# Kernel tuning notes

Measured on AMD Instinct MI355X. Metric: run time of the kernel, lower is better.

## Reference

```python
import jax, jax.numpy as jnp
import numpy as np

B, T, I, H, O = 64, 2048, 128, 512, 128


def setup_inputs() -> dict:
    key = jax.random.key(0)
    ks = jax.random.split(key, 9)
    sI = 1.0 / np.sqrt(I)
    sH = 1.0 / np.sqrt(H)
    return {
        "x": jax.random.normal(ks[0], (B, T, I), jnp.float32),
        "h0": jnp.zeros((1, B, H), jnp.float32),
        "W_ih": jax.random.normal(ks[1], (H, I), jnp.float32) * sI,
        "b_ih": jax.random.normal(ks[2], (H,), jnp.float32) * sH,
        "W_hh": jax.random.normal(ks[3], (H, H), jnp.float32) * sH,
        "b_hh": jax.random.normal(ks[4], (H,), jnp.float32) * sH,
        "mask_ih": (jax.random.uniform(ks[5], (H, I)) < 0.8).astype(jnp.float32),
        "mask_hh": (jax.random.uniform(ks[6], (H, H)) < 0.8).astype(jnp.float32),
        "W_fc": jax.random.normal(ks[7], (O, H), jnp.float32) * sH,
        "b_fc": jax.random.normal(ks[8], (O,), jnp.float32) * sH,
    }


def reference(x, h0, W_ih, b_ih, W_hh, b_hh, mask_ih, mask_hh, W_fc, b_fc):
    # Masked weights (mask applied once, outside the time loop)
    Wih_m = W_ih * mask_ih          # [H, I]
    Whh_m = W_hh * mask_hh          # [H, H]

    # Precompute the input projection for all timesteps: [T, B, H]
    xt = jnp.swapaxes(x, 0, 1)      # time-major for scan
    xproj = jnp.einsum("tbi,hi->tbh", xt, Wih_m) + b_ih + b_hh

    def step(h, xp_t):
        # Elman RNN cell with tanh nonlinearity (torch nn.RNN default)
        h_new = jnp.tanh(xp_t + h @ Whh_m.T)
        return h_new, h_new

    _, hs = jax.lax.scan(step, h0[0], xproj)   # hs: [T, B, H]

    # Linear readout over all timesteps, back to batch_first
    out = jnp.einsum("tbh,oh->tbo", hs, W_fc) + b_fc
    return jnp.swapaxes(out, 0, 1)             # [B, T, O]
```

## Files before the change

### kernel.cpp

```cpp
#include <hip/hip_runtime.h>

typedef unsigned int u32;
typedef _Float16 half_t;
typedef _Float16 half2_t __attribute__((ext_vector_type(2)));

#define B_ 64
#define T_ 2048
#define I_ 128
#define H_ 512
#define O_ 128

static __device__ __forceinline__ float dot2w(u32 w, u32 h, float acc) {
  return __builtin_amdgcn_fdot2(__builtin_bit_cast(half2_t, w),
                                __builtin_bit_cast(half2_t, h), acc, false);
}

__global__ void k_prep(const float* __restrict__ Whh, const float* __restrict__ Mhh,
                       const float* __restrict__ Wih, const float* __restrict__ Mih,
                       const float* __restrict__ Wfc,
                       u32* __restrict__ Whh_pk, u32* __restrict__ Wih_pk,
                       u32* __restrict__ Wfc_pk) {
  int idx = blockIdx.x * 256 + threadIdx.x;
  if (idx < 512 * 256) {
    int w4 = idx >> 11;
    int rem = idx & 2047;
    int l = rem >> 2;
    int c = rem & 3;
    int q = w4 * 4 + c;
    int j = q >> 5;
    int m = q & 31;
    int row = (l >> 3) * 8 + j;
    int k0 = (l & 7) * 64 + m * 2;
    float a = Whh[row * 512 + k0]     * Mhh[row * 512 + k0];
    float b = Whh[row * 512 + k0 + 1] * Mhh[row * 512 + k0 + 1];
    half2_t hv = { (half_t)a, (half_t)b };
    Whh_pk[idx] = __builtin_bit_cast(u32, hv);
  } else if (idx < 512 * 256 + 512 * 64) {
    int i2 = idx - 512 * 256;
    int h = i2 >> 6, w = i2 & 63;
    int k0 = w * 2;
    float a = Wih[h * 128 + k0]     * Mih[h * 128 + k0];
    float b = Wih[h * 128 + k0 + 1] * Mih[h * 128 + k0 + 1];
    half2_t hv = { (half_t)a, (half_t)b };
    Wih_pk[h * 64 + w] = __builtin_bit_cast(u32, hv);
  } else if (idx < 512 * 256 + 512 * 64 + 128 * 256) {
    int i3 = idx - (512 * 256 + 512 * 64);
    int o = i3 >> 8, w = i3 & 255;
    float a = Wfc[o * 512 + 2 * w];
    float b = Wfc[o * 512 + 2 * w + 1];
    half2_t hv = { (half_t)a, (half_t)b };
    Wfc_pk[o * 256 + w] = __builtin_bit_cast(u32, hv);
  }
}

__launch_bounds__(512, 2)
__global__ void k_xproj(const float* __restrict__ x, const u32* __restrict__ Wih_pk,
                        const float* __restrict__ b_ih, const float* __restrict__ b_hh,
                        half_t* __restrict__ xp) {
  const int l = threadIdx.x;
  const int r0 = blockIdx.x * 256;
  __shared__ u32 xb[2][64];
  u32 W[64];
#pragma unroll
  for (int i = 0; i < 16; ++i)
    *(uint4*)&W[i * 4] = *(const uint4*)(Wih_pk + l * 64 + i * 4);
  const float bs = b_ih[l] + b_hh[l];

  float2 g = { 0.f, 0.f };
  if (l < 64) {
    g = *(const float2*)(x + (size_t)r0 * 128 + 2 * l);
    half2_t hv = { (half_t)g.x, (half_t)g.y };
    xb[0][l] = __builtin_bit_cast(u32, hv);
    g = *(const float2*)(x + (size_t)(r0 + 1) * 128 + 2 * l);
  }
  __syncthreads();
  for (int i = 0; i < 256; ++i) {
    if (l < 64 && i + 1 < 256) {
      half2_t hv = { (half_t)g.x, (half_t)g.y };
      xb[(i + 1) & 1][l] = __builtin_bit_cast(u32, hv);
      int nf = (i + 2 < 256) ? i + 2 : i + 1;
      g = *(const float2*)(x + (size_t)(r0 + nf) * 128 + 2 * l);
    }
    float a0 = 0.f, a1 = 0.f;
#pragma unroll
    for (int m = 0; m < 16; ++m) {
      uint4 hv = *(const uint4*)&xb[i & 1][m * 4];
      a0 = dot2w(W[m * 4 + 0], hv.x, a0);
      a1 = dot2w(W[m * 4 + 1], hv.y, a1);
      a0 = dot2w(W[m * 4 + 2], hv.z, a0);
      a1 = dot2w(W[m * 4 + 3], hv.w, a1);
    }
    xp[(size_t)(r0 + i) * 512 + l] = (half_t)(a0 + a1 + bs);
    __syncthreads();
  }
}

__launch_bounds__(512, 2)
__global__ void k_rec(const u32* __restrict__ Whh_pk, half_t* __restrict__ xp,
                      const float* __restrict__ h0) {
  const int b = blockIdx.x;
  const int l = threadIdx.x;
  const int g = l & 7;
  const int row = l;

  __shared__ u32 hbuf[2][288];
  __shared__ u32 wlds[512 * 52];

  u32 W[208];
#pragma unroll
  for (int w4 = 0; w4 < 64; ++w4) {
    uint4 v = *(const uint4*)(Whh_pk + (size_t)w4 * 2048 + l * 4);
    const int j = w4 >> 3, p = w4 & 7;
    if (j < 4) {
      if (p < 7) {
        W[j * 28 + p * 4 + 0] = v.x; W[j * 28 + p * 4 + 1] = v.y;
        W[j * 28 + p * 4 + 2] = v.z; W[j * 28 + p * 4 + 3] = v.w;
      } else {
        *(uint4*)&wlds[l * 52 + j * 4] = v;
      }
    } else {
      if (p < 6) {
        int base = 112 + (j - 4) * 24 + p * 4;
        W[base + 0] = v.x; W[base + 1] = v.y; W[base + 2] = v.z; W[base + 3] = v.w;
      } else {
        *(uint4*)&wlds[l * 52 + 16 + (j - 4) * 8 + (p - 6) * 4] = v;
      }
    }
  }
  if (l < 256) {
    float2 hv = *(const float2*)(h0 + (size_t)b * 512 + 2 * l);
    half2_t hh = { (half_t)hv.x, (half_t)hv.y };
    hbuf[0][l + (l >> 5) * 4] = __builtin_bit_cast(u32, hh);
  }
  __syncthreads();

  half_t* xpb = xp + (size_t)b * T_ * 512 + row;
  half_t xp0 = xpb[0];
  half_t xp1 = xpb[512];

  const int b0 = l & 1, b1 = (l >> 1) & 1, b2 = (l >> 2) & 1;
  const int hwIdx = (row >> 1) + (row >> 6) * 4;
  int cur = 0;

  for (int t = 0; t < T_; ++t) {
    int tpf = (t + 2 < T_) ? t + 2 : T_ - 1;
    half_t xpn = xpb[(size_t)tpf * 512];

    float acc[8];
#pragma unroll
    for (int j = 0; j < 8; ++j) acc[j] = 0.f;

#pragma unroll
    for (int m4 = 0; m4 < 8; ++m4) {
      uint4 hh = *(const uint4*)&hbuf[cur][g * 36 + m4 * 4];
#pragma unroll
      for (int j = 0; j < 8; ++j) {
        u32 w0, w1, w2, w3;
        if (j < 4) {
          if (m4 < 7) {
            w0 = W[j * 28 + m4 * 4 + 0]; w1 = W[j * 28 + m4 * 4 + 1];
            w2 = W[j * 28 + m4 * 4 + 2]; w3 = W[j * 28 + m4 * 4 + 3];
          } else {
            uint4 wv = *(const uint4*)&wlds[l * 52 + j * 4];
            w0 = wv.x; w1 = wv.y; w2 = wv.z; w3 = wv.w;
          }
        } else {
          if (m4 < 6) {
            int base = 112 + (j - 4) * 24 + m4 * 4;
            w0 = W[base + 0]; w1 = W[base + 1]; w2 = W[base + 2]; w3 = W[base + 3];
          } else {
            uint4 wv = *(const uint4*)&wlds[l * 52 + 16 + (j - 4) * 8 + (m4 - 6) * 4];
            w0 = wv.x; w1 = wv.y; w2 = wv.z; w3 = wv.w;
          }
        }
        acc[j] = dot2w(w0, hh.x, acc[j]);
        acc[j] = dot2w(w1, hh.y, acc[j]);
        acc[j] = dot2w(w2, hh.z, acc[j]);
        acc[j] = dot2w(w3, hh.w, acc[j]);
      }
    }

    float s4[4];
#pragma unroll
    for (int m = 0; m < 4; ++m) {
      float keep = b0 ? acc[2 * m + 1] : acc[2 * m];
      float send = b0 ? acc[2 * m]     : acc[2 * m + 1];
      s4[m] = keep + __shfl_xor(send, 1, 64);
    }
    float s2[2];
#pragma unroll
    for (int m = 0; m < 2; ++m) {
      float keep = b1 ? s4[2 * m + 1] : s4[2 * m];
      float send = b1 ? s4[2 * m]     : s4[2 * m + 1];
      s2[m] = keep + __shfl_xor(send, 2, 64);
    }
    float keepf = b2 ? s2[1] : s2[0];
    float sendf = b2 ? s2[0] : s2[1];
    float tot = keepf + __shfl_xor(sendf, 4, 64);

    float sarg = tot + (float)xp0;
    float ax = fabsf(sarg);
    float e = __expf(-2.f * ax);
    float r = (1.f - e) * __builtin_amdgcn_rcpf(1.f + e);
    float hval = copysignf(r, sarg);

    half_t hv = (half_t)hval;
    ((half_t*)hbuf[cur ^ 1])[hwIdx * 2 + (row & 1)] = hv;
    xpb[(size_t)t * 512] = hv;

    xp0 = xp1; xp1 = xpn;
    __syncthreads();
    cur ^= 1;
  }
}

__launch_bounds__(256, 2)
__global__ void k_fc(const half_t* __restrict__ hs, const u32* __restrict__ Wfc_pk,
                     const float* __restrict__ b_fc, float* __restrict__ out) {
  const int l = threadIdx.x;
  const int w = l >> 6;
  const int o = (l & 31) + w * 32;
  const int kh = (l >> 5) & 1;
  const int r0 = blockIdx.x * 256;
  __shared__ u32 sb[2][256];
  u32 W[128];
#pragma unroll
  for (int i = 0; i < 32; ++i)
    *(uint4*)&W[i * 4] = *(const uint4*)(Wfc_pk + o * 256 + kh * 128 + i * 4);
  const float bf = b_fc[o];
  const u32* hsw = (const u32*)hs;

  u32 gA = hsw[(size_t)r0 * 256 + l];
  sb[0][l] = gA;
  gA = hsw[(size_t)(r0 + 1) * 256 + l];
  __syncthreads();
  for (int i = 0; i < 256; ++i) {
    if (i + 1 < 256) {
      sb[(i + 1) & 1][l] = gA;
      int nf = (i + 2 < 256) ? i + 2 : i + 1;
      gA = hsw[(size_t)(r0 + nf) * 256 + l];
    }
    float a0 = 0.f, a1 = 0.f;
#pragma unroll
    for (int m = 0; m < 32; ++m) {
      uint4 hv = *(const uint4*)&sb[i & 1][kh * 128 + m * 4];
      a0 = dot2w(W[m * 4 + 0], hv.x, a0);
      a1 = dot2w(W[m * 4 + 1], hv.y, a1);
      a0 = dot2w(W[m * 4 + 2], hv.z, a0);
      a1 = dot2w(W[m * 4 + 3], hv.w, a1);
    }
    float a = a0 + a1;
    a += __shfl_xor(a, 32, 64);
    if (kh == 0) out[(size_t)(r0 + i) * 128 + o] = a + bf;
    __syncthreads();
  }
}

extern "C" void kernel_launch(void* const* d_in, const int* in_sizes, int n_in,
                              void* d_out, int out_size, void* d_ws, size_t ws_size,
                              hipStream_t stream) {
  const float* x   = (const float*)d_in[0];
  const float* h0  = (const float*)d_in[1];
  const float* Wih = (const float*)d_in[2];
  const float* bih = (const float*)d_in[3];
  const float* Whh = (const float*)d_in[4];
  const float* bhh = (const float*)d_in[5];
  const float* Mih = (const float*)d_in[6];
  const float* Mhh = (const float*)d_in[7];
  const float* Wfc = (const float*)d_in[8];
  const float* bfc = (const float*)d_in[9];
  float* out = (float*)d_out;

  char* ws = (char*)d_ws;
  half_t* xproj = (half_t*)(ws);
  u32* Whh_pk = (u32*)(ws + 134217728);
  u32* Wih_pk = (u32*)(ws + 134217728 + 524288);
  u32* Wfc_pk = (u32*)(ws + 134217728 + 524288 + 131072);

  hipLaunchKernelGGL(k_prep, dim3(768), dim3(256), 0, stream,
                     Whh, Mhh, Wih, Mih, Wfc, Whh_pk, Wih_pk, Wfc_pk);
  hipLaunchKernelGGL(k_xproj, dim3(512), dim3(512), 0, stream,
                     x, Wih_pk, bih, bhh, xproj);
  hipLaunchKernelGGL(k_rec, dim3(64), dim3(512), 0, stream,
                     Whh_pk, xproj, h0);
  hipLaunchKernelGGL(k_fc, dim3(512), dim3(256), 0, stream,
                     xproj, Wfc_pk, bfc, out);
}
```

Before: 3.404 ms.

## Stream part of recurrent weights from global/L2 each step instead of LDS

The recurrent kernel keeps 160 words of W_hh per thread in registers and drops the LDS-resident portion. The remaining three weight column blocks are reloaded from global memory (L2-cached) on every timestep, software-pipelined behind the register-resident dot products with scheduling barriers. Launch bounds change from 2 to 1 blocks per CU. This removes the large LDS footprint and LDS weight reads, but adds per-step global loads whose latency sits on the serial recurrence critical path.

Measured after the change: 5.006 ms. 1.47x slower.

```diff
diff --git a/kernel.cpp b/kernel.cpp
--- a/kernel.cpp
+++ b/kernel.cpp
@@ -95,38 +95,25 @@
   }
 }
 
-__launch_bounds__(512, 2)
+__launch_bounds__(512, 1)
 __global__ void k_rec(const u32* __restrict__ Whh_pk, half_t* __restrict__ xp,
                       const float* __restrict__ h0) {
   const int b = blockIdx.x;
   const int l = threadIdx.x;
   const int g = l & 7;
-  const int row = l;
 
   __shared__ u32 hbuf[2][288];
-  __shared__ u32 wlds[512 * 52];
-
-  u32 W[208];
-#pragma unroll
-  for (int w4 = 0; w4 < 64; ++w4) {
-    uint4 v = *(const uint4*)(Whh_pk + (size_t)w4 * 2048 + l * 4);
-    const int j = w4 >> 3, p = w4 & 7;
-    if (j < 4) {
-      if (p < 7) {
-        W[j * 28 + p * 4 + 0] = v.x; W[j * 28 + p * 4 + 1] = v.y;
-        W[j * 28 + p * 4 + 2] = v.z; W[j * 28 + p * 4 + 3] = v.w;
-      } else {
-        *(uint4*)&wlds[l * 52 + j * 4] = v;
-      }
-    } else {
-      if (p < 6) {
-        int base = 112 + (j - 4) * 24 + p * 4;
-        W[base + 0] = v.x; W[base + 1] = v.y; W[base + 2] = v.z; W[base + 3] = v.w;
-      } else {
-        *(uint4*)&wlds[l * 52 + 16 + (j - 4) * 8 + (p - 6) * 4] = v;
-      }
-    }
-  }
+
+  u32 W[160];
+#pragma unroll
+  for (int j = 0; j < 8; ++j)
+#pragma unroll
+    for (int m4 = 0; m4 < 5; ++m4) {
+      uint4 v = *(const uint4*)(Whh_pk + (size_t)(j * 8 + m4) * 2048 + l * 4);
+      W[j * 20 + m4 * 4 + 0] = v.x; W[j * 20 + m4 * 4 + 1] = v.y;
+      W[j * 20 + m4 * 4 + 2] = v.z; W[j * 20 + m4 * 4 + 3] = v.w;
+    }
+
   if (l < 256) {
     float2 hv = *(const float2*)(h0 + (size_t)b * 512 + 2 * l);
     half2_t hh = { (half_t)hv.x, (half_t)hv.y };
@@ -134,15 +121,23 @@
   }
   __syncthreads();
 
-  half_t* xpb = xp + (size_t)b * T_ * 512 + row;
+  const uint4* wstream = (const uint4*)Whh_pk + l;
+
+  half_t* xpb = xp + (size_t)b * T_ * 512 + l;
   half_t xp0 = xpb[0];
   half_t xp1 = xpb[512];
 
   const int b0 = l & 1, b1 = (l >> 1) & 1, b2 = (l >> 2) & 1;
-  const int hwIdx = (row >> 1) + (row >> 6) * 4;
+  const int hwIdx = (l >> 1) + (l >> 6) * 4;
   int cur = 0;
 
   for (int t = 0; t < T_; ++t) {
+    const uint4* p5 = wstream;
+    asm volatile("" : "+v"(p5));
+    uint4 L5[8];
+#pragma unroll
+    for (int j = 0; j < 8; ++j) L5[j] = p5[(j * 8 + 5) * 512];
+
     int tpf = (t + 2 < T_) ? t + 2 : T_ - 1;
     half_t xpn = xpb[(size_t)tpf * 512];
 
@@ -151,32 +146,58 @@
     for (int j = 0; j < 8; ++j) acc[j] = 0.f;
 
 #pragma unroll
-    for (int m4 = 0; m4 < 8; ++m4) {
+    for (int m4 = 0; m4 < 5; ++m4) {
       uint4 hh = *(const uint4*)&hbuf[cur][g * 36 + m4 * 4];
 #pragma unroll
       for (int j = 0; j < 8; ++j) {
-        u32 w0, w1, w2, w3;
-        if (j < 4) {
-          if (m4 < 7) {
-            w0 = W[j * 28 + m4 * 4 + 0]; w1 = W[j * 28 + m4 * 4 + 1];
-            w2 = W[j * 28 + m4 * 4 + 2]; w3 = W[j * 28 + m4 * 4 + 3];
-          } else {
-            uint4 wv = *(const uint4*)&wlds[l * 52 + j * 4];
-            w0 = wv.x; w1 = wv.y; w2 = wv.z; w3 = wv.w;
-          }
-        } else {
-          if (m4 < 6) {
-            int base = 112 + (j - 4) * 24 + m4 * 4;
-            w0 = W[base + 0]; w1 = W[base + 1]; w2 = W[base + 2]; w3 = W[base + 3];
-          } else {
-            uint4 wv = *(const uint4*)&wlds[l * 52 + 16 + (j - 4) * 8 + (m4 - 6) * 4];
-            w0 = wv.x; w1 = wv.y; w2 = wv.z; w3 = wv.w;
-          }
-        }
-        acc[j] = dot2w(w0, hh.x, acc[j]);
-        acc[j] = dot2w(w1, hh.y, acc[j]);
-        acc[j] = dot2w(w2, hh.z, acc[j]);
-        acc[j] = dot2w(w3, hh.w, acc[j]);
+        acc[j] = dot2w(W[j * 20 + m4 * 4 + 0], hh.x, acc[j]);
+        acc[j] = dot2w(W[j * 20 + m4 * 4 + 1], hh.y, acc[j]);
+        acc[j] = dot2w(W[j * 20 + m4 * 4 + 2], hh.z, acc[j]);
+        acc[j] = dot2w(W[j * 20 + m4 * 4 + 3], hh.w, acc[j]);
+      }
+    }
+
+    __builtin_amdgcn_sched_barrier(0);
+    const uint4* p6 = wstream;
+    asm volatile("" : "+v"(p6));
+    uint4 L6[8];
+#pragma unroll
+    for (int j = 0; j < 8; ++j) L6[j] = p6[(j * 8 + 6) * 512];
+    {
+      uint4 hh = *(const uint4*)&hbuf[cur][g * 36 + 20];
+#pragma unroll
+      for (int j = 0; j < 8; ++j) {
+        acc[j] = dot2w(L5[j].x, hh.x, acc[j]);
+        acc[j] = dot2w(L5[j].y, hh.y, acc[j]);
+        acc[j] = dot2w(L5[j].z, hh.z, acc[j]);
+        acc[j] = dot2w(L5[j].w, hh.w, acc[j]);
+      }
+    }
+
+    __builtin_amdgcn_sched_barrier(0);
+    const uint4* p7 = wstream;
+    asm volatile("" : "+v"(p7));
+    uint4 L7[8];
+#pragma unroll
+    for (int j = 0; j < 8; ++j) L7[j] = p7[(j * 8 + 7) * 512];
+    {
+      uint4 hh = *(const uint4*)&hbuf[cur][g * 36 + 24];
+#pragma unroll
+      for (int j = 0; j < 8; ++j) {
+        acc[j] = dot2w(L6[j].x, hh.x, acc[j]);
+        acc[j] = dot2w(L6[j].y, hh.y, acc[j]);
+        acc[j] = dot2w(L6[j].z, hh.z, acc[j]);
+        acc[j] = dot2w(L6[j].w, hh.w, acc[j]);
+      }
+    }
+    {
+      uint4 hh = *(const uint4*)&hbuf[cur][g * 36 + 28];
+#pragma unroll
+      for (int j = 0; j < 8; ++j) {
+        acc[j] = dot2w(L7[j].x, hh.x, acc[j]);
+        acc[j] = dot2w(L7[j].y, hh.y, acc[j]);
+        acc[j] = dot2w(L7[j].z, hh.z, acc[j]);
+        acc[j] = dot2w(L7[j].w, hh.w, acc[j]);
       }
     }
 
@@ -205,7 +226,7 @@
     float hval = copysignf(r, sarg);
 
     half_t hv = (half_t)hval;
-    ((half_t*)hbuf[cur ^ 1])[hwIdx * 2 + (row & 1)] = hv;
+    ((half_t*)hbuf[cur ^ 1])[hwIdx * 2 + (l & 1)] = hv;
     xpb[(size_t)t * 512] = hv;
 
     xp0 = xp1; xp1 = xpn;
```

## Stream spilled recurrent weights from global/L2 with software prefetch instead of LDS

Applied to the files above, without the earlier changes.

The recurrent kernel now keeps 45 weight blocks pinned in registers through named variables and asm barriers. It drops the LDS copy of the remaining weights. Those 19 blocks are reloaded from global memory (L2-resident) every timestep, with loads issued one block ahead of their use so they overlap the dot-product chain. Launch bounds go from 2 blocks to 1 block per CU, so each thread can hold more registers. The risk is extra L2 traffic and latency on every step of the serial recurrence, plus lower occupancy, in exchange for freeing LDS and removing the compiler's weight-array handling.

Measured after the change: 4.613 ms. 35.5% more time.

```diff
diff --git a/kernel.cpp b/kernel.cpp
--- a/kernel.cpp
+++ b/kernel.cpp
@@ -95,38 +95,48 @@
   }
 }
 
-__launch_bounds__(512, 2)
+#define WPLD(N, J, M4) u32 N##_x, N##_y, N##_z, N##_w; \
+  { uint4 t_ = wpk4[((J) * 8 + (M4)) * 512 + l]; \
+    N##_x = t_.x; N##_y = t_.y; N##_z = t_.z; N##_w = t_.w; }
+#define DECLROW(J) WPLD(W##J##_0, J, 0) WPLD(W##J##_1, J, 1) WPLD(W##J##_2, J, 2) \
+                   WPLD(W##J##_3, J, 3) WPLD(W##J##_4, J, 4) WPLD(W##J##_5, J, 5) \
+                   WPLD(W##J##_6, J, 6) WPLD(W##J##_7, J, 7)
+#define LNDF(N) asm volatile("" : "+v"(N##_x), "+v"(N##_y), "+v"(N##_z), "+v"(N##_w));
+#define LNDROW(J) LNDF(W##J##_0) LNDF(W##J##_1) LNDF(W##J##_2) LNDF(W##J##_3) \
+                  LNDF(W##J##_4) LNDF(W##J##_5) LNDF(W##J##_6) LNDF(W##J##_7)
+#define DOTR(Jn, N) { acc[Jn] = dot2w(N##_x, hh.x, acc[Jn]); acc[Jn] = dot2w(N##_y, hh.y, acc[Jn]); \
+                      acc[Jn] = dot2w(N##_z, hh.z, acc[Jn]); acc[Jn] = dot2w(N##_w, hh.w, acc[Jn]); }
+#define DOTU(Jn, V) { acc[Jn] = dot2w((V).x, hh.x, acc[Jn]); acc[Jn] = dot2w((V).y, hh.y, acc[Jn]); \
+                      acc[Jn] = dot2w((V).z, hh.z, acc[Jn]); acc[Jn] = dot2w((V).w, hh.w, acc[Jn]); }
+#define ISS2(M) const uint4* p##M = wst; asm volatile("" : "+v"(p##M)); \
+  uint4 s6_##M = p##M[(48 + M) * 512]; uint4 s7_##M = p##M[(56 + M) * 512];
+#define ISS3(M) const uint4* p##M = wst; asm volatile("" : "+v"(p##M)); \
+  uint4 s5_##M = p##M[(40 + M) * 512]; uint4 s6_##M = p##M[(48 + M) * 512]; \
+  uint4 s7_##M = p##M[(56 + M) * 512];
+#define BLK_A(M) { uint4 hh = *(const uint4*)&hbc[g * 36 + M * 4]; \
+  DOTR(0, W0_##M) DOTR(1, W1_##M) DOTR(2, W2_##M) DOTR(3, W3_##M) DOTR(4, W4_##M) \
+  DOTR(5, W5_##M) DOTU(6, s6_##M) DOTU(7, s7_##M) }
+#define BLK_B(M) { uint4 hh = *(const uint4*)&hbc[g * 36 + M * 4]; \
+  DOTR(0, W0_##M) DOTR(1, W1_##M) DOTR(2, W2_##M) DOTR(3, W3_##M) DOTR(4, W4_##M) \
+  DOTU(5, s5_##M) DOTU(6, s6_##M) DOTU(7, s7_##M) }
+
+__launch_bounds__(512, 1)
 __global__ void k_rec(const u32* __restrict__ Whh_pk, half_t* __restrict__ xp,
                       const float* __restrict__ h0) {
   const int b = blockIdx.x;
   const int l = threadIdx.x;
   const int g = l & 7;
-  const int row = l;
 
   __shared__ u32 hbuf[2][288];
-  __shared__ u32 wlds[512 * 52];
-
-  u32 W[208];
-#pragma unroll
-  for (int w4 = 0; w4 < 64; ++w4) {
-    uint4 v = *(const uint4*)(Whh_pk + (size_t)w4 * 2048 + l * 4);
-    const int j = w4 >> 3, p = w4 & 7;
-    if (j < 4) {
-      if (p < 7) {
-        W[j * 28 + p * 4 + 0] = v.x; W[j * 28 + p * 4 + 1] = v.y;
-        W[j * 28 + p * 4 + 2] = v.z; W[j * 28 + p * 4 + 3] = v.w;
-      } else {
-        *(uint4*)&wlds[l * 52 + j * 4] = v;
-      }
-    } else {
-      if (p < 6) {
-        int base = 112 + (j - 4) * 24 + p * 4;
-        W[base + 0] = v.x; W[base + 1] = v.y; W[base + 2] = v.z; W[base + 3] = v.w;
-      } else {
-        *(uint4*)&wlds[l * 52 + 16 + (j - 4) * 8 + (p - 6) * 4] = v;
-      }
-    }
-  }
+
+  const uint4* wpk4 = (const uint4*)Whh_pk;
+
+  DECLROW(0) DECLROW(1) DECLROW(2) DECLROW(3) DECLROW(4)
+  WPLD(W5_0, 5, 0) WPLD(W5_1, 5, 1) WPLD(W5_2, 5, 2) WPLD(W5_3, 5, 3) WPLD(W5_4, 5, 4)
+
+  LNDROW(0) LNDROW(1) LNDROW(2) LNDROW(3) LNDROW(4)
+  LNDF(W5_0) LNDF(W5_1) LNDF(W5_2) LNDF(W5_3) LNDF(W5_4)
+
   if (l < 256) {
     float2 hv = *(const float2*)(h0 + (size_t)b * 512 + 2 * l);
     half2_t hh = { (half_t)hv.x, (half_t)hv.y };
@@ -134,15 +144,21 @@
   }
   __syncthreads();
 
-  half_t* xpb = xp + (size_t)b * T_ * 512 + row;
+  const uint4* wst = wpk4 + l;
+
+  half_t* xpb = xp + (size_t)b * T_ * 512 + l;
   half_t xp0 = xpb[0];
   half_t xp1 = xpb[512];
 
   const int b0 = l & 1, b1 = (l >> 1) & 1, b2 = (l >> 2) & 1;
-  const int hwIdx = (row >> 1) + (row >> 6) * 4;
+  const int hwIdx = (l >> 1) + (l >> 6) * 4;
   int cur = 0;
 
   for (int t = 0; t < T_; ++t) {
+    const u32* hbc = hbuf[cur];
+
+    ISS2(0) ISS2(1)
+
     int tpf = (t + 2 < T_) ? t + 2 : T_ - 1;
     half_t xpn = xpb[(size_t)tpf * 512];
 
@@ -150,35 +166,14 @@
 #pragma unroll
     for (int j = 0; j < 8; ++j) acc[j] = 0.f;
 
-#pragma unroll
-    for (int m4 = 0; m4 < 8; ++m4) {
-      uint4 hh = *(const uint4*)&hbuf[cur][g * 36 + m4 * 4];
-#pragma unroll
-      for (int j = 0; j < 8; ++j) {
-        u32 w0, w1, w2, w3;
-        if (j < 4) {
-          if (m4 < 7) {
-            w0 = W[j * 28 + m4 * 4 + 0]; w1 = W[j * 28 + m4 * 4 + 1];
-            w2 = W[j * 28 + m4 * 4 + 2]; w3 = W[j * 28 + m4 * 4 + 3];
-          } else {
-            uint4 wv = *(const uint4*)&wlds[l * 52 + j * 4];
-            w0 = wv.x; w1 = wv.y; w2 = wv.z; w3 = wv.w;
-          }
-        } else {
-          if (m4 < 6) {
-            int base = 112 + (j - 4) * 24 + m4 * 4;
-            w0 = W[base + 0]; w1 = W[base + 1]; w2 = W[base + 2]; w3 = W[base + 3];
-          } else {
-            uint4 wv = *(const uint4*)&wlds[l * 52 + 16 + (j - 4) * 8 + (m4 - 6) * 4];
-            w0 = wv.x; w1 = wv.y; w2 = wv.z; w3 = wv.w;
-          }
-        }
-        acc[j] = dot2w(w0, hh.x, acc[j]);
-        acc[j] = dot2w(w1, hh.y, acc[j]);
-        acc[j] = dot2w(w2, hh.z, acc[j]);
-        acc[j] = dot2w(w3, hh.w, acc[j]);
-      }
-    }
+    BLK_A(0) ISS2(2)
+    BLK_A(1) ISS2(3)
+    BLK_A(2) ISS2(4)
+    BLK_A(3) ISS3(5)
+    BLK_A(4) ISS3(6)
+    BLK_B(5) ISS3(7)
+    BLK_B(6)
+    BLK_B(7)
 
     float s4[4];
 #pragma unroll
@@ -205,7 +200,7 @@
     float hval = copysignf(r, sarg);
 
     half_t hv = (half_t)hval;
-    ((half_t*)hbuf[cur ^ 1])[hwIdx * 2 + (row & 1)] = hv;
+    ((half_t*)hbuf[cur ^ 1])[hwIdx * 2 + (l & 1)] = hv;
     xpb[(size_t)t * 512] = hv;
 
     xp0 = xp1; xp1 = xpn;
```
